# Performance work log

Hardware: AMD Instinct MI355X
Metric: run time of the kernel (lower is better)

## Reference

```python
import jax, jax.numpy as jnp
import numpy as np

N = 50000      # nodes
E = 800000     # edges
G = 64         # graphs in batch
H = 256        # hidden_channels
CE = 128       # coord embed dim = H//2
OTH = 6        # in_channels - 3
ED = 8         # edge_dim
EE = 128       # edge_embedding_dim
GD = 16        # global_dim
L = 3          # num_layers


def setup_inputs() -> dict:
    key = jax.random.key(0)
    ks = jax.random.split(key, 24)
    s = 0.05
    inp = {
        "x": jax.random.normal(ks[0], (N, 9), jnp.float32),
        "edge_index": jax.random.randint(ks[1], (2, E), 0, N),
        "batch": jnp.sort(jax.random.randint(ks[2], (N,), 0, G)),
        "edge_attr": jax.random.normal(ks[3], (E, ED), jnp.float32),
        "global_x": jax.random.normal(ks[4], (G, GD), jnp.float32),
        # coordinate embedder (Linear 3->128 + relu)
        "coord_W": jax.random.normal(ks[5], (3, CE), jnp.float32) * s,
        "coord_b": jnp.zeros((CE,), jnp.float32),
        # node_mlp (Linear 6->128 + relu)
        "node_W": jax.random.normal(ks[6], (OTH, CE), jnp.float32) * s,
        "node_b": jnp.zeros((CE,), jnp.float32),
        # edge processor (Linear 8->128 + relu) and projection 128->256
        "edge_W": jax.random.normal(ks[7], (ED, EE), jnp.float32) * s,
        "edge_b": jnp.zeros((EE,), jnp.float32),
        "proj_W": jax.random.normal(ks[8], (EE, H), jnp.float32) * s,
        "proj_b": jnp.zeros((H,), jnp.float32),
        # stacked GCN layer weights
        "gcn_W": jax.random.normal(ks[9], (L, H, H), jnp.float32) * s,
        "gcn_b": jnp.zeros((L, H), jnp.float32),
        # attention pooling
        "attn_w": jax.random.normal(ks[10], (H,), jnp.float32) * s,
        "attn_b": jnp.zeros((), jnp.float32),
        # global_mlp: Linear 16->256, relu, Linear 256->256
        "gmlp_W1": jax.random.normal(ks[11], (GD, H), jnp.float32) * s,
        "gmlp_b1": jnp.zeros((H,), jnp.float32),
        "gmlp_W2": jax.random.normal(ks[12], (H, H), jnp.float32) * s,
        "gmlp_b2": jnp.zeros((H,), jnp.float32),
        # fc_out: Linear 512->256, relu, Linear 256->1
        "fc_W1": jax.random.normal(ks[13], (2 * H, H), jnp.float32) * s,
        "fc_b1": jnp.zeros((H,), jnp.float32),
        "fc_W2": jax.random.normal(ks[14], (H, 1), jnp.float32) * s,
        "fc_b2": jnp.zeros((1,), jnp.float32),
    }
    return inp


def _segsum(v, idx, num):
    return jax.ops.segment_sum(v, idx, num_segments=num)


def reference(x, edge_index, batch, edge_attr, global_x,
              coord_W, coord_b, node_W, node_b, edge_W, edge_b,
              proj_W, proj_b, gcn_W, gcn_b, attn_w, attn_b,
              gmlp_W1, gmlp_b1, gmlp_W2, gmlp_b2,
              fc_W1, fc_b1, fc_W2, fc_b2):
    relu = jax.nn.relu
    # --- node embedding: coords + other features ---
    coord_emb = relu(x[:, :3] @ coord_W + coord_b)          # [N, 128]
    other_emb = relu(x[:, 3:] @ node_W + node_b)            # [N, 128]
    x_emb = jnp.concatenate([coord_emb, other_emb], axis=1)  # [N, 256]

    # --- edge embedding, aggregated to target nodes (index_add over col) ---
    edge_emb = relu(edge_attr @ edge_W + edge_b) @ proj_W + proj_b  # [E, 256]
    col0 = edge_index[1]
    node_msg = _segsum(edge_emb, col0, N)                    # [N, 256]

    # --- GCN normalization with self-loops ---
    sl = jnp.arange(N)
    row = jnp.concatenate([edge_index[0], sl])
    col = jnp.concatenate([edge_index[1], sl])
    deg = _segsum(jnp.ones_like(col, jnp.float32), col, N)   # >= 1
    dnorm = jax.lax.rsqrt(deg)
    efac = (dnorm[row] * dnorm[col])[:, None]                # [E+N, 1]

    # --- stacked GCN layers (edge messages re-added each layer, per source) ---
    for i in range(L):
        x_in = x_emb + node_msg
        h = x_in @ gcn_W[i]                                  # [N, 256]
        x_emb = _segsum(h[row] * efac, col, N) + gcn_b[i]
        if i < L - 1:
            x_emb = relu(x_emb)

    # --- attention pooling (per-graph softmax over batch index) ---
    scores = x_emb @ attn_w + attn_b                         # [N]
    m = jax.ops.segment_max(scores, batch, num_segments=G)
    e = jnp.exp(scores - m[batch])
    denom = _segsum(e, batch, G)
    attn = e / denom[batch]
    graph_emb = _segsum(x_emb * attn[:, None], batch, G)     # [G, 256]

    # --- global features + head ---
    g = relu(global_x @ gmlp_W1 + gmlp_b1) @ gmlp_W2 + gmlp_b2
    hcat = jnp.concatenate([graph_emb, g], axis=-1)          # [G, 512]
    out = relu(hcat @ fc_W1 + fc_b1) @ fc_W2 + fc_b2         # [G, 1]
    return out
```

## Files before the change

kernel.cpp:

```cpp
#include <hip/hip_runtime.h>


typedef float f32x4 __attribute__((ext_vector_type(4)));
typedef short s16x8 __attribute__((ext_vector_type(8)));

__device__ __forceinline__ unsigned short f2bf(float f) {
  union { float f; unsigned u; } v{f};
  unsigned r = v.u + 0x7fff + ((v.u >> 16) & 1);
  return (unsigned short)(r >> 16);
}
__device__ __forceinline__ float bf2f(unsigned short s) {
  union { unsigned u; float f; } v{(unsigned)s << 16};
  return v.f;
}
__device__ __forceinline__ float blo(unsigned u) {
  union { unsigned x; float f; } v{u << 16};
  return v.f;
}
__device__ __forceinline__ float bhi(unsigned u) {
  union { unsigned x; float f; } v{u & 0xffff0000u};
  return v.f;
}
__device__ __forceinline__ unsigned pk2(float a, float b) {
  return (unsigned)f2bf(a) | ((unsigned)f2bf(b) << 16);
}

__global__ void node_embed_kernel(const float* __restrict__ x,
                                  const float* __restrict__ coord_W, const float* __restrict__ coord_b,
                                  const float* __restrict__ node_W, const float* __restrict__ node_b,
                                  short* __restrict__ x0, int N) {
  int tid = threadIdx.x;
  int node = blockIdx.x * 8 + (tid >> 5);
  if (node >= N) return;
  int ch0 = (tid & 31) * 8;
  const float* xr = x + (size_t)node * 9;
  float a[8];
  if (ch0 < 128) {
    float4 b0 = *(const float4*)&coord_b[ch0];
    float4 b1 = *(const float4*)&coord_b[ch0 + 4];
    a[0]=b0.x; a[1]=b0.y; a[2]=b0.z; a[3]=b0.w; a[4]=b1.x; a[5]=b1.y; a[6]=b1.z; a[7]=b1.w;
#pragma unroll
    for (int k = 0; k < 3; k++) {
      float xv = xr[k];
      float4 w0 = *(const float4*)&coord_W[k * 128 + ch0];
      float4 w1 = *(const float4*)&coord_W[k * 128 + ch0 + 4];
      a[0] = fmaf(xv, w0.x, a[0]); a[1] = fmaf(xv, w0.y, a[1]);
      a[2] = fmaf(xv, w0.z, a[2]); a[3] = fmaf(xv, w0.w, a[3]);
      a[4] = fmaf(xv, w1.x, a[4]); a[5] = fmaf(xv, w1.y, a[5]);
      a[6] = fmaf(xv, w1.z, a[6]); a[7] = fmaf(xv, w1.w, a[7]);
    }
  } else {
    int c0 = ch0 - 128;
    float4 b0 = *(const float4*)&node_b[c0];
    float4 b1 = *(const float4*)&node_b[c0 + 4];
    a[0]=b0.x; a[1]=b0.y; a[2]=b0.z; a[3]=b0.w; a[4]=b1.x; a[5]=b1.y; a[6]=b1.z; a[7]=b1.w;
#pragma unroll
    for (int k = 0; k < 6; k++) {
      float xv = xr[3 + k];
      float4 w0 = *(const float4*)&node_W[k * 128 + c0];
      float4 w1 = *(const float4*)&node_W[k * 128 + c0 + 4];
      a[0] = fmaf(xv, w0.x, a[0]); a[1] = fmaf(xv, w0.y, a[1]);
      a[2] = fmaf(xv, w0.z, a[2]); a[3] = fmaf(xv, w0.w, a[3]);
      a[4] = fmaf(xv, w1.x, a[4]); a[5] = fmaf(xv, w1.y, a[5]);
      a[6] = fmaf(xv, w1.z, a[6]); a[7] = fmaf(xv, w1.w, a[7]);
    }
  }
  uint4 o;
  o.x = pk2(fmaxf(a[0], 0.f), fmaxf(a[1], 0.f));
  o.y = pk2(fmaxf(a[2], 0.f), fmaxf(a[3], 0.f));
  o.z = pk2(fmaxf(a[4], 0.f), fmaxf(a[5], 0.f));
  o.w = pk2(fmaxf(a[6], 0.f), fmaxf(a[7], 0.f));
  *(uint4*)&x0[(size_t)node * 256 + ch0] = o;
}

__global__ void count_kernel(const int* __restrict__ col, int* __restrict__ cnt, int E) {
  int e = blockIdx.x * 256 + threadIdx.x;
  if (e < E) atomicAdd(&cnt[col[e]], 1);
}

__global__ void breduce_kernel(const int* __restrict__ cnt, int* __restrict__ partials, int N) {
  __shared__ int red[256];
  int t = threadIdx.x;
  int i = blockIdx.x * 256 + t;
  int v = (i < N) ? cnt[i] : 0;
  red[t] = v;
  __syncthreads();
  for (int off = 128; off; off >>= 1) {
    if (t < off) red[t] += red[t + off];
    __syncthreads();
  }
  if (t == 0) partials[blockIdx.x] = red[0];
}

__global__ void scan_partials_kernel(int* __restrict__ partials, int nb) {
  __shared__ int s[1024];
  int t = threadIdx.x;
  for (int i = t; i < nb; i += 256) s[i] = partials[i];
  __syncthreads();
  if (t == 0) {
    int run = 0;
    for (int i = 0; i < nb; i++) { int c = s[i]; s[i] = run; run += c; }
  }
  __syncthreads();
  for (int i = t; i < nb; i += 256) partials[i] = s[i];
}

__global__ void scan_apply_kernel(const int* __restrict__ cnt, const int* __restrict__ partials,
                                  int* __restrict__ rowstart, float* __restrict__ dnorm,
                                  int* __restrict__ cursor, int N) {
  __shared__ int red[256];
  int t = threadIdx.x;
  int i = blockIdx.x * 256 + t;
  int v = (i < N) ? cnt[i] : 0;
  red[t] = v;
  __syncthreads();
  for (int off = 1; off < 256; off <<= 1) {
    int x = (t >= off) ? red[t - off] : 0;
    __syncthreads();
    red[t] += x;
    __syncthreads();
  }
  if (i < N) {
    int ex = red[t] - v + partials[blockIdx.x];
    rowstart[i] = ex;
    dnorm[i] = rsqrtf((float)(v + 1));
    cursor[i] = 0;
    if (i == N - 1) rowstart[N] = ex + v;
  }
}

__global__ void scatter_kernel(const int* __restrict__ row, const int* __restrict__ col,
                               const float* __restrict__ edge_attr,
                               const int* __restrict__ rowstart, int* __restrict__ cursor,
                               const float* __restrict__ dnorm,
                               int* __restrict__ csr_row, float* __restrict__ csr_efac,
                               float* __restrict__ ea_sorted, int E) {
  int e = blockIdx.x * 256 + threadIdx.x;
  if (e >= E) return;
  int c = col[e], r = row[e];
  int p = atomicAdd(&cursor[c], 1);
  int slot = rowstart[c] + p;
  csr_row[slot] = r;
  csr_efac[slot] = dnorm[r] * dnorm[c];
  const float4* src = (const float4*)(edge_attr + (size_t)e * 8);
  float4* dst = (float4*)(ea_sorted + (size_t)slot * 8);
  float4 s0 = src[0], s1 = src[1];
  dst[0] = s0;
  dst[1] = s1;
}

__global__ void wt_kernel(const float* __restrict__ gcn_W, const float* __restrict__ proj_W,
                          short* __restrict__ gcnWt, short* __restrict__ projWt) {
  int idx = blockIdx.x * 256 + threadIdx.x;
  if (idx < 3 * 65536) {
    int l = idx >> 16, r = idx & 65535, n = r >> 8, k = r & 255;
    gcnWt[idx] = (short)f2bf(gcn_W[l * 65536 + k * 256 + n]);
  } else {
    int j = idx - 3 * 65536;
    int n = j >> 7, k = j & 127;
    projWt[j] = (short)f2bf(proj_W[k * 256 + n]);
  }
}

__global__ void edge_msg_kernel(const float* __restrict__ ea_sorted,
                                const int* __restrict__ rowstart,
                                const float* __restrict__ edge_W, const float* __restrict__ edge_b,
                                short* __restrict__ msg128, int N) {
  int node = blockIdx.x;
  int ch = threadIdx.x;
  __shared__ float sW[8 * 128];
  __shared__ float sb[128];
  for (int i = ch; i < 8 * 128; i += 128) sW[i] = edge_W[i];
  sb[ch] = edge_b[ch];
  __syncthreads();
  float acc = 0.f;
  int s0 = rowstart[node], s1 = rowstart[node + 1];
  const float4* ea4 = (const float4*)ea_sorted;
  for (int s = s0; s < s1; s++) {
    float4 e0 = ea4[(size_t)s * 2];
    float4 e1 = ea4[(size_t)s * 2 + 1];
    float t = sb[ch];
    t = fmaf(e0.x, sW[0 * 128 + ch], t);
    t = fmaf(e0.y, sW[1 * 128 + ch], t);
    t = fmaf(e0.z, sW[2 * 128 + ch], t);
    t = fmaf(e0.w, sW[3 * 128 + ch], t);
    t = fmaf(e1.x, sW[4 * 128 + ch], t);
    t = fmaf(e1.y, sW[5 * 128 + ch], t);
    t = fmaf(e1.z, sW[6 * 128 + ch], t);
    t = fmaf(e1.w, sW[7 * 128 + ch], t);
    acc += fmaxf(t, 0.f);
  }
  msg128[(size_t)node * 128 + ch] = (short)f2bf(acc);
}

__global__ void __launch_bounds__(256) proj_gemm_mfma(
    const short* __restrict__ msg128, const short* __restrict__ projWt,
    const float* __restrict__ proj_b, const int* __restrict__ cnt,
    const short* __restrict__ x0, float* __restrict__ node_msg,
    short* __restrict__ xin0, int N) {
  __shared__ short As[64][136];
  int tid = threadIdx.x;
  int n0 = blockIdx.x * 64;
  for (int i = tid; i < 64 * 32; i += 256) {
    int r = i >> 5, c4 = (i & 31) << 2;
    int n = n0 + r;
    uint2 v = make_uint2(0, 0);
    if (n < N) v = *(const uint2*)&msg128[(size_t)n * 128 + c4];
    *(uint2*)&As[r][c4] = v;
  }
  __syncthreads();
  int wave = tid >> 6, lane = tid & 63;
  int mrow = wave * 16 + (lane & 15);
  int kgrp = (lane >> 4) * 8;
  f32x4 acc[16];
#pragma unroll
  for (int i = 0; i < 16; i++) acc[i] = (f32x4){0.f, 0.f, 0.f, 0.f};
  const short* wbase = projWt + (size_t)(lane & 15) * 128 + kgrp;
#pragma unroll
  for (int kk = 0; kk < 4; kk++) {
    s16x8 a = *(const s16x8*)&As[mrow][kk * 32 + kgrp];
#pragma unroll
    for (int nf = 0; nf < 16; nf++) {
      s16x8 b = *(const s16x8*)&wbase[(size_t)nf * 16 * 128 + kk * 32];
      acc[nf] = __builtin_amdgcn_mfma_f32_16x16x32_bf16(a, b, acc[nf], 0, 0, 0);
    }
  }
  int orow0 = wave * 16 + (lane >> 4) * 4;
  int ocol = lane & 15;
#pragma unroll
  for (int nf = 0; nf < 16; nf++) {
    int c = nf * 16 + ocol;
    float pb = proj_b[c];
#pragma unroll
    for (int r = 0; r < 4; r++) {
      int n = n0 + orow0 + r;
      if (n < N) {
        float v = acc[nf][r] + (float)cnt[n] * pb;
        node_msg[(size_t)n * 256 + c] = v;
        xin0[(size_t)n * 256 + c] =
            (short)f2bf(v + bf2f((unsigned short)x0[(size_t)n * 256 + c]));
      }
    }
  }
}

__global__ void __launch_bounds__(256) gcn_gemm_mfma(
    const short* __restrict__ Xin, const short* __restrict__ Wt,
    short* __restrict__ Hout, int N) {
  __shared__ short As[64][264];
  int tid = threadIdx.x;
  int n0 = blockIdx.x * 64;
  for (int i = tid; i < 64 * 64; i += 256) {
    int r = i >> 6, c4 = (i & 63) << 2;
    int n = n0 + r;
    uint2 v = make_uint2(0, 0);
    if (n < N) v = *(const uint2*)&Xin[(size_t)n * 256 + c4];
    *(uint2*)&As[r][c4] = v;
  }
  __syncthreads();
  int wave = tid >> 6, lane = tid & 63;
  int mrow = wave * 16 + (lane & 15);
  int kgrp = (lane >> 4) * 8;
  f32x4 acc[16];
#pragma unroll
  for (int i = 0; i < 16; i++) acc[i] = (f32x4){0.f, 0.f, 0.f, 0.f};
  const short* wbase = Wt + (size_t)(lane & 15) * 256 + kgrp;
#pragma unroll
  for (int kk = 0; kk < 8; kk++) {
    s16x8 a = *(const s16x8*)&As[mrow][kk * 32 + kgrp];
#pragma unroll
    for (int nf = 0; nf < 16; nf++) {
      s16x8 b = *(const s16x8*)&wbase[(size_t)nf * 16 * 256 + kk * 32];
      acc[nf] = __builtin_amdgcn_mfma_f32_16x16x32_bf16(a, b, acc[nf], 0, 0, 0);
    }
  }
  int orow0 = wave * 16 + (lane >> 4) * 4;
  int ocol = lane & 15;
#pragma unroll
  for (int nf = 0; nf < 16; nf++) {
#pragma unroll
    for (int r = 0; r < 4; r++) {
      int n = n0 + orow0 + r;
      if (n < N) Hout[(size_t)n * 256 + nf * 16 + ocol] = (short)f2bf(acc[nf][r]);
    }
  }
}

__global__ void __launch_bounds__(256) gcn_agg_kernel(
    const short* __restrict__ h, const int* __restrict__ csr_row,
    const float* __restrict__ csr_efac, const int* __restrict__ rowstart,
    const float* __restrict__ dnorm, const float* __restrict__ b,
    const float* __restrict__ node_msg, short* __restrict__ xin,
    float* __restrict__ x_emb, const float* __restrict__ attn_w,
    const float* __restrict__ attn_b, float* __restrict__ scores,
    int last, int N) {
  int lane = threadIdx.x & 63;
  int node = blockIdx.x * 4 + (threadIdx.x >> 6);
  if (node >= N) return;
  int ch0 = lane << 2;
  size_t rowb = (size_t)node * 256 + ch0;
  float dn = dnorm[node];
  float w = dn * dn;
  uint2 hv = *(const uint2*)&h[rowb];
  float a0 = blo(hv.x) * w, a1 = bhi(hv.x) * w;
  float a2 = blo(hv.y) * w, a3 = bhi(hv.y) * w;
  int s = rowstart[node], s1 = rowstart[node + 1];
  for (; s + 4 <= s1; s += 4) {
    int r0 = csr_row[s], r1 = csr_row[s + 1], r2 = csr_row[s + 2], r3 = csr_row[s + 3];
    float f0 = csr_efac[s], f1 = csr_efac[s + 1], f2 = csr_efac[s + 2], f3 = csr_efac[s + 3];
    uint2 v0 = *(const uint2*)&h[(size_t)r0 * 256 + ch0];
    uint2 v1 = *(const uint2*)&h[(size_t)r1 * 256 + ch0];
    uint2 v2 = *(const uint2*)&h[(size_t)r2 * 256 + ch0];
    uint2 v3 = *(const uint2*)&h[(size_t)r3 * 256 + ch0];
    a0 = fmaf(blo(v0.x), f0, a0); a1 = fmaf(bhi(v0.x), f0, a1);
    a2 = fmaf(blo(v0.y), f0, a2); a3 = fmaf(bhi(v0.y), f0, a3);
    a0 = fmaf(blo(v1.x), f1, a0); a1 = fmaf(bhi(v1.x), f1, a1);
    a2 = fmaf(blo(v1.y), f1, a2); a3 = fmaf(bhi(v1.y), f1, a3);
    a0 = fmaf(blo(v2.x), f2, a0); a1 = fmaf(bhi(v2.x), f2, a1);
    a2 = fmaf(blo(v2.y), f2, a2); a3 = fmaf(bhi(v2.y), f2, a3);
    a0 = fmaf(blo(v3.x), f3, a0); a1 = fmaf(bhi(v3.x), f3, a1);
    a2 = fmaf(blo(v3.y), f3, a2); a3 = fmaf(bhi(v3.y), f3, a3);
  }
  for (; s < s1; s++) {
    int r = csr_row[s];
    float f = csr_efac[s];
    uint2 v = *(const uint2*)&h[(size_t)r * 256 + ch0];
    a0 = fmaf(blo(v.x), f, a0); a1 = fmaf(bhi(v.x), f, a1);
    a2 = fmaf(blo(v.y), f, a2); a3 = fmaf(bhi(v.y), f, a3);
  }
  float4 bv = *(const float4*)&b[ch0];
  a0 += bv.x; a1 += bv.y; a2 += bv.z; a3 += bv.w;
  if (!last) {
    float4 mv = *(const float4*)&node_msg[rowb];
    float y0 = fmaxf(a0, 0.f) + mv.x;
    float y1 = fmaxf(a1, 0.f) + mv.y;
    float y2 = fmaxf(a2, 0.f) + mv.z;
    float y3 = fmaxf(a3, 0.f) + mv.w;
    uint2 o;
    o.x = pk2(y0, y1);
    o.y = pk2(y2, y3);
    *(uint2*)&xin[rowb] = o;
  } else {
    *(float4*)&x_emb[rowb] = make_float4(a0, a1, a2, a3);
    float4 aw = *(const float4*)&attn_w[ch0];
    float p = a0 * aw.x + a1 * aw.y + a2 * aw.z + a3 * aw.w;
#pragma unroll
    for (int off = 32; off; off >>= 1) p += __shfl_down(p, off);
    if (lane == 0) scores[node] = p + attn_b[0];
  }
}

__global__ void gse_kernel(const int* __restrict__ batch, int* __restrict__ gs,
                           int* __restrict__ ge, int N) {
  int i = blockIdx.x * 256 + threadIdx.x;
  if (i >= N) return;
  int g = batch[i];
  if (i == 0) gs[g] = 0;
  else {
    int gp = batch[i - 1];
    if (gp != g) { gs[g] = i; ge[gp] = i - 1; }
  }
  if (i == N - 1) ge[g] = N - 1;
}

__global__ void softmax_kernel(const float* __restrict__ scores, const int* __restrict__ gs,
                               const int* __restrict__ ge, float* __restrict__ wnode) {
  int g = blockIdx.x;
  int tid = threadIdx.x;
  __shared__ float red[256];
  int s0 = gs[g], e1 = ge[g];
  if (s0 > e1) return;
  int s1 = e1 + 1;
  float m = -1e30f;
  for (int i = s0 + tid; i < s1; i += 256) m = fmaxf(m, scores[i]);
  red[tid] = m;
  __syncthreads();
  for (int off = 128; off; off >>= 1) {
    if (tid < off) red[tid] = fmaxf(red[tid], red[tid + off]);
    __syncthreads();
  }
  m = red[0];
  __syncthreads();
  float d = 0.f;
  for (int i = s0 + tid; i < s1; i += 256) d += expf(scores[i] - m);
  red[tid] = d;
  __syncthreads();
  for (int off = 128; off; off >>= 1) {
    if (tid < off) red[tid] += red[tid + off];
    __syncthreads();
  }
  float rd = 1.f / red[0];
  for (int i = s0 + tid; i < s1; i += 256) wnode[i] = expf(scores[i] - m) * rd;
}

__global__ void __launch_bounds__(256) pool_sum_kernel(
    const float* __restrict__ x_emb, const float* __restrict__ wnode,
    const int* __restrict__ batch, float* __restrict__ graph_emb, int N) {
  __shared__ int sb[256];
  __shared__ float sw[256];
  int ch = threadIdx.x;
  int i0 = blockIdx.x * 256;
  int lim = min(256, N - i0);
  if (ch < lim) { sb[ch] = batch[i0 + ch]; sw[ch] = wnode[i0 + ch]; }
  __syncthreads();
  int curg = sb[0];
  float acc = 0.f;
  for (int j = 0; j < lim; j++) {
    int g = sb[j];
    if (g != curg) {
      atomicAdd(&graph_emb[(size_t)curg * 256 + ch], acc);
      acc = 0.f;
      curg = g;
    }
    acc = fmaf(x_emb[(size_t)(i0 + j) * 256 + ch], sw[j], acc);
  }
  atomicAdd(&graph_emb[(size_t)curg * 256 + ch], acc);
}

__global__ void head_kernel(const float* __restrict__ global_x, const float* __restrict__ graph_emb,
                            const float* __restrict__ W1, const float* __restrict__ b1,
                            const float* __restrict__ W2, const float* __restrict__ b2,
                            const float* __restrict__ fW1, const float* __restrict__ fb1,
                            const float* __restrict__ fW2, const float* __restrict__ fb2,
                            float* __restrict__ out) {
  int g = blockIdx.x;
  int ch = threadIdx.x;
  __shared__ float t1[256], g2s[256], t3s[256];
  float a = b1[ch];
  const float* gx = global_x + g * 16;
#pragma unroll
  for (int k = 0; k < 16; k++) a = fmaf(gx[k], W1[k * 256 + ch], a);
  t1[ch] = fmaxf(a, 0.f);
  __syncthreads();
  float bb = b2[ch];
  for (int k = 0; k < 256; k++) bb = fmaf(t1[k], W2[k * 256 + ch], bb);
  g2s[ch] = bb;
  __syncthreads();
  float c = fb1[ch];
  const float* ger = graph_emb + (size_t)g * 256;
  for (int k = 0; k < 256; k++) c = fmaf(ger[k], fW1[k * 256 + ch], c);
  for (int k = 0; k < 256; k++) c = fmaf(g2s[k], fW1[(256 + k) * 256 + ch], c);
  t3s[ch] = fmaxf(c, 0.f);
  __syncthreads();
  t1[ch] = t3s[ch] * fW2[ch];
  __syncthreads();
  for (int off = 128; off; off >>= 1) {
    if (ch < off) t1[ch] += t1[ch + off];
    __syncthreads();
  }
  if (ch == 0) out[g] = t1[0] + fb2[0];
}

extern "C" void kernel_launch(void* const* d_in, const int* in_sizes, int n_in,
                              void* d_out, int out_size, void* d_ws, size_t ws_size,
                              hipStream_t stream) {
  const float* x        = (const float*)d_in[0];
  const int*   ei       = (const int*)d_in[1];
  const int*   batch    = (const int*)d_in[2];
  const float* edge_attr= (const float*)d_in[3];
  const float* global_x = (const float*)d_in[4];
  const float* coord_W  = (const float*)d_in[5];
  const float* coord_b  = (const float*)d_in[6];
  const float* node_W   = (const float*)d_in[7];
  const float* node_b   = (const float*)d_in[8];
  const float* edge_W   = (const float*)d_in[9];
  const float* edge_b   = (const float*)d_in[10];
  const float* proj_W   = (const float*)d_in[11];
  const float* proj_b   = (const float*)d_in[12];
  const float* gcn_W    = (const float*)d_in[13];
  const float* gcn_b    = (const float*)d_in[14];
  const float* attn_w   = (const float*)d_in[15];
  const float* attn_b   = (const float*)d_in[16];
  const float* gmlp_W1  = (const float*)d_in[17];
  const float* gmlp_b1  = (const float*)d_in[18];
  const float* gmlp_W2  = (const float*)d_in[19];
  const float* gmlp_b2  = (const float*)d_in[20];
  const float* fc_W1    = (const float*)d_in[21];
  const float* fc_b1    = (const float*)d_in[22];
  const float* fc_W2    = (const float*)d_in[23];
  const float* fc_b2    = (const float*)d_in[24];

  const int N = in_sizes[0] / 9;
  const int E = in_sizes[3] / 8;
  const int G = in_sizes[4] / 16;
  const int NB = (N + 255) / 256;

  char* w = (char*)d_ws;
  auto alloc = [&](size_t bytes) -> char* {
    char* p = w;
    w += (bytes + 255) & ~(size_t)255;
    return p;
  };
  float* node_msg = (float*)alloc((size_t)N * 256 * 4);
  short* xin      = (short*)alloc((size_t)N * 256 * 2);
  short* h        = (short*)alloc((size_t)N * 256 * 2);
  short* x0       = (short*)alloc((size_t)N * 256 * 2);
  float* big      = (float*)alloc((size_t)N * 256 * 4);
  short* msg128   = h;
  float* ea_sorted= big;
  float* x_emb    = big;
  short* gcnWt    = (short*)alloc((size_t)3 * 65536 * 2);
  short* projWt   = (short*)alloc((size_t)256 * 128 * 2);
  int*   cnt      = (int*)alloc((size_t)N * 4);
  int*   rowstart = (int*)alloc((size_t)(N + 1) * 4);
  int*   cursor   = (int*)alloc((size_t)N * 4);
  float* dnorm    = (float*)alloc((size_t)N * 4);
  int*   csr_row  = (int*)alloc((size_t)E * 4);
  float* csr_efac = (float*)alloc((size_t)E * 4);
  float* scores   = (float*)alloc((size_t)N * 4);
  float* wnode    = (float*)alloc((size_t)N * 4);
  int*   partials = (int*)alloc((size_t)NB * 4);
  int*   gs       = (int*)alloc((size_t)G * 4);
  int*   ge       = (int*)alloc((size_t)G * 4);
  float* graph_emb= (float*)alloc((size_t)G * 256 * 4);

  hipMemsetAsync(cnt, 0, (size_t)N * 4, stream);
  hipMemsetAsync(gs, 0x7f, (size_t)G * 4, stream);
  hipMemsetAsync(ge, 0xff, (size_t)G * 4, stream);
  hipMemsetAsync(graph_emb, 0, (size_t)G * 256 * 4, stream);

  wt_kernel<<<(3 * 65536 + 256 * 128 + 255) / 256, 256, 0, stream>>>(gcn_W, proj_W, gcnWt, projWt);
  node_embed_kernel<<<(N + 7) / 8, 256, 0, stream>>>(
      x, coord_W, coord_b, node_W, node_b, x0, N);
  count_kernel<<<(E + 255) / 256, 256, 0, stream>>>(ei + E, cnt, E);
  breduce_kernel<<<NB, 256, 0, stream>>>(cnt, partials, N);
  scan_partials_kernel<<<1, 256, 0, stream>>>(partials, NB);
  scan_apply_kernel<<<NB, 256, 0, stream>>>(cnt, partials, rowstart, dnorm, cursor, N);
  scatter_kernel<<<(E + 255) / 256, 256, 0, stream>>>(
      ei, ei + E, edge_attr, rowstart, cursor, dnorm, csr_row, csr_efac, ea_sorted, E);
  edge_msg_kernel<<<N, 128, 0, stream>>>(ea_sorted, rowstart, edge_W, edge_b, msg128, N);
  proj_gemm_mfma<<<(N + 63) / 64, 256, 0, stream>>>(
      msg128, projWt, proj_b, cnt, x0, node_msg, xin, N);
  for (int l = 0; l < 3; l++) {
    gcn_gemm_mfma<<<(N + 63) / 64, 256, 0, stream>>>(
        xin, gcnWt + (size_t)l * 65536, h, N);
    gcn_agg_kernel<<<(N + 3) / 4, 256, 0, stream>>>(
        h, csr_row, csr_efac, rowstart, dnorm, gcn_b + (size_t)l * 256,
        node_msg, xin, x_emb, attn_w, attn_b, scores, (l == 2) ? 1 : 0, N);
  }
  gse_kernel<<<(N + 255) / 256, 256, 0, stream>>>(batch, gs, ge, N);
  softmax_kernel<<<G, 256, 0, stream>>>(scores, gs, ge, wnode);
  pool_sum_kernel<<<NB, 256, 0, stream>>>(x_emb, wnode, batch, graph_emb, N);
  head_kernel<<<G, 256, 0, stream>>>(global_x, graph_emb, gmlp_W1, gmlp_b1, gmlp_W2, gmlp_b2,
                                     fc_W1, fc_b1, fc_W2, fc_b2, (float*)d_out);
}
```

Baseline: 957.5 us.

## Fuse GCN aggregation into next layer's GEMM and pack CSR edge records

Each GCN layer's neighbor aggregation, bias, relu and node-message add now fills the shared-memory A tile that feeds the next layer's MFMA GEMM. The first GCN GEMM is folded into the projection kernel, which removes the round trip of the xin activation through global memory and cuts launches. CSR edge data is packed into one int4 record (edge id, source, norm factor), and edge_msg now gathers edge_attr by id instead of reading a presorted copy. node_msg and x_emb are stored as bf16, lowering bandwidth at some precision cost. The fused layer kernel runs the aggregation with 64-node blocks where each wave walks 16 nodes serially, so parallelism and latency hiding during the gather may drop.

```diff
diff --git a/kernel.cpp b/kernel.cpp
--- a/kernel.cpp
+++ b/kernel.cpp
@@ -130,23 +130,15 @@
 }
 
 __global__ void scatter_kernel(const int* __restrict__ row, const int* __restrict__ col,
-                               const float* __restrict__ edge_attr,
                                const int* __restrict__ rowstart, int* __restrict__ cursor,
                                const float* __restrict__ dnorm,
-                               int* __restrict__ csr_row, float* __restrict__ csr_efac,
-                               float* __restrict__ ea_sorted, int E) {
+                               int4* __restrict__ pk, int E) {
   int e = blockIdx.x * 256 + threadIdx.x;
   if (e >= E) return;
   int c = col[e], r = row[e];
   int p = atomicAdd(&cursor[c], 1);
   int slot = rowstart[c] + p;
-  csr_row[slot] = r;
-  csr_efac[slot] = dnorm[r] * dnorm[c];
-  const float4* src = (const float4*)(edge_attr + (size_t)e * 8);
-  float4* dst = (float4*)(ea_sorted + (size_t)slot * 8);
-  float4 s0 = src[0], s1 = src[1];
-  dst[0] = s0;
-  dst[1] = s1;
+  pk[slot] = make_int4(e, r, __float_as_int(dnorm[r] * dnorm[c]), 0);
 }
 
 __global__ void wt_kernel(const float* __restrict__ gcn_W, const float* __restrict__ proj_W,
@@ -162,7 +154,8 @@
   }
 }
 
-__global__ void edge_msg_kernel(const float* __restrict__ ea_sorted,
+__global__ void edge_msg_kernel(const float* __restrict__ edge_attr,
+                                const int4* __restrict__ pk,
                                 const int* __restrict__ rowstart,
                                 const float* __restrict__ edge_W, const float* __restrict__ edge_b,
                                 short* __restrict__ msg128, int N) {
@@ -175,10 +168,10 @@
   __syncthreads();
   float acc = 0.f;
   int s0 = rowstart[node], s1 = rowstart[node + 1];
-  const float4* ea4 = (const float4*)ea_sorted;
   for (int s = s0; s < s1; s++) {
-    float4 e0 = ea4[(size_t)s * 2];
-    float4 e1 = ea4[(size_t)s * 2 + 1];
+    int eid = pk[s].x;
+    const float4* ea = (const float4*)(edge_attr + (size_t)eid * 8);
+    float4 e0 = ea[0], e1 = ea[1];
     float t = sb[ch];
     t = fmaf(e0.x, sW[0 * 128 + ch], t);
     t = fmaf(e0.y, sW[1 * 128 + ch], t);
@@ -193,12 +186,13 @@
   msg128[(size_t)node * 128 + ch] = (short)f2bf(acc);
 }
 
-__global__ void __launch_bounds__(256) proj_gemm_mfma(
+__global__ void __launch_bounds__(256) fused_proj_gemm(
     const short* __restrict__ msg128, const short* __restrict__ projWt,
     const float* __restrict__ proj_b, const int* __restrict__ cnt,
-    const short* __restrict__ x0, float* __restrict__ node_msg,
-    short* __restrict__ xin0, int N) {
+    const short* __restrict__ x0, const short* __restrict__ W0t,
+    short* __restrict__ node_msg, short* __restrict__ hout, int N) {
   __shared__ short As[64][136];
+  __shared__ short Xs[64][264];
   int tid = threadIdx.x;
   int n0 = blockIdx.x * 64;
   for (int i = tid; i < 64 * 32; i += 256) {
@@ -215,50 +209,123 @@
   f32x4 acc[16];
 #pragma unroll
   for (int i = 0; i < 16; i++) acc[i] = (f32x4){0.f, 0.f, 0.f, 0.f};
-  const short* wbase = projWt + (size_t)(lane & 15) * 128 + kgrp;
-#pragma unroll
-  for (int kk = 0; kk < 4; kk++) {
-    s16x8 a = *(const s16x8*)&As[mrow][kk * 32 + kgrp];
-#pragma unroll
-    for (int nf = 0; nf < 16; nf++) {
-      s16x8 b = *(const s16x8*)&wbase[(size_t)nf * 16 * 128 + kk * 32];
-      acc[nf] = __builtin_amdgcn_mfma_f32_16x16x32_bf16(a, b, acc[nf], 0, 0, 0);
+  {
+    const short* wbase = projWt + (size_t)(lane & 15) * 128 + kgrp;
+#pragma unroll
+    for (int kk = 0; kk < 4; kk++) {
+      s16x8 a = *(const s16x8*)&As[mrow][kk * 32 + kgrp];
+#pragma unroll
+      for (int nf = 0; nf < 16; nf++) {
+        s16x8 b = *(const s16x8*)&wbase[(size_t)nf * 16 * 128 + kk * 32];
+        acc[nf] = __builtin_amdgcn_mfma_f32_16x16x32_bf16(a, b, acc[nf], 0, 0, 0);
+      }
     }
   }
   int orow0 = wave * 16 + (lane >> 4) * 4;
   int ocol = lane & 15;
 #pragma unroll
+  for (int r = 0; r < 4; r++) {
+    int i = orow0 + r;
+    int n = n0 + i;
+    if (n < N) {
+      float cn = (float)cnt[n];
+#pragma unroll
+      for (int nf = 0; nf < 16; nf++) {
+        int c = nf * 16 + ocol;
+        float v = acc[nf][r] + cn * proj_b[c];
+        unsigned short nm = f2bf(v);
+        node_msg[(size_t)n * 256 + c] = (short)nm;
+        Xs[i][c] = (short)f2bf(bf2f(nm) + bf2f((unsigned short)x0[(size_t)n * 256 + c]));
+      }
+    } else {
+#pragma unroll
+      for (int nf = 0; nf < 16; nf++) Xs[i][nf * 16 + ocol] = 0;
+    }
+  }
+  __syncthreads();
+#pragma unroll
+  for (int i = 0; i < 16; i++) acc[i] = (f32x4){0.f, 0.f, 0.f, 0.f};
+  {
+    const short* wbase = W0t + (size_t)(lane & 15) * 256 + kgrp;
+#pragma unroll
+    for (int kk = 0; kk < 8; kk++) {
+      s16x8 a = *(const s16x8*)&Xs[mrow][kk * 32 + kgrp];
+#pragma unroll
+      for (int nf = 0; nf < 16; nf++) {
+        s16x8 b = *(const s16x8*)&wbase[(size_t)nf * 16 * 256 + kk * 32];
+        acc[nf] = __builtin_amdgcn_mfma_f32_16x16x32_bf16(a, b, acc[nf], 0, 0, 0);
+      }
+    }
+  }
+#pragma unroll
   for (int nf = 0; nf < 16; nf++) {
-    int c = nf * 16 + ocol;
-    float pb = proj_b[c];
 #pragma unroll
     for (int r = 0; r < 4; r++) {
       int n = n0 + orow0 + r;
-      if (n < N) {
-        float v = acc[nf][r] + (float)cnt[n] * pb;
-        node_msg[(size_t)n * 256 + c] = v;
-        xin0[(size_t)n * 256 + c] =
-            (short)f2bf(v + bf2f((unsigned short)x0[(size_t)n * 256 + c]));
-      }
-    }
-  }
-}
-
-__global__ void __launch_bounds__(256) gcn_gemm_mfma(
-    const short* __restrict__ Xin, const short* __restrict__ Wt,
-    short* __restrict__ Hout, int N) {
-  __shared__ short As[64][264];
+      if (n < N) hout[(size_t)n * 256 + nf * 16 + ocol] = (short)f2bf(acc[nf][r]);
+    }
+  }
+}
+
+__global__ void __launch_bounds__(256) fused_layer(
+    const short* __restrict__ hprev, const int4* __restrict__ pk,
+    const int* __restrict__ rowstart, const float* __restrict__ dnorm,
+    const float* __restrict__ bprev, const short* __restrict__ node_msg,
+    const short* __restrict__ Wt, short* __restrict__ hnext, int N) {
+  __shared__ short Xs[64][264];
   int tid = threadIdx.x;
   int n0 = blockIdx.x * 64;
-  for (int i = tid; i < 64 * 64; i += 256) {
-    int r = i >> 6, c4 = (i & 63) << 2;
-    int n = n0 + r;
-    uint2 v = make_uint2(0, 0);
-    if (n < N) v = *(const uint2*)&Xin[(size_t)n * 256 + c4];
-    *(uint2*)&As[r][c4] = v;
-  }
-  __syncthreads();
   int wave = tid >> 6, lane = tid & 63;
+  int ch0 = lane << 2;
+  float4 bv = *(const float4*)&bprev[ch0];
+  for (int i = wave * 16; i < wave * 16 + 16; i++) {
+    int n = n0 + i;
+    if (n >= N) {
+      *(uint2*)&Xs[i][ch0] = make_uint2(0, 0);
+      continue;
+    }
+    size_t rowb = (size_t)n * 256 + ch0;
+    float dn = dnorm[n];
+    float wgt = dn * dn;
+    uint2 hv = *(const uint2*)&hprev[rowb];
+    float a0 = blo(hv.x) * wgt, a1 = bhi(hv.x) * wgt;
+    float a2 = blo(hv.y) * wgt, a3 = bhi(hv.y) * wgt;
+    int s = rowstart[n], s1 = rowstart[n + 1];
+    for (; s + 4 <= s1; s += 4) {
+      int4 p0 = pk[s], p1 = pk[s + 1], p2 = pk[s + 2], p3 = pk[s + 3];
+      float f0 = __int_as_float(p0.z), f1 = __int_as_float(p1.z);
+      float f2 = __int_as_float(p2.z), f3 = __int_as_float(p3.z);
+      uint2 v0 = *(const uint2*)&hprev[(size_t)p0.y * 256 + ch0];
+      uint2 v1 = *(const uint2*)&hprev[(size_t)p1.y * 256 + ch0];
+      uint2 v2 = *(const uint2*)&hprev[(size_t)p2.y * 256 + ch0];
+      uint2 v3 = *(const uint2*)&hprev[(size_t)p3.y * 256 + ch0];
+      a0 = fmaf(blo(v0.x), f0, a0); a1 = fmaf(bhi(v0.x), f0, a1);
+      a2 = fmaf(blo(v0.y), f0, a2); a3 = fmaf(bhi(v0.y), f0, a3);
+      a0 = fmaf(blo(v1.x), f1, a0); a1 = fmaf(bhi(v1.x), f1, a1);
+      a2 = fmaf(blo(v1.y), f1, a2); a3 = fmaf(bhi(v1.y), f1, a3);
+      a0 = fmaf(blo(v2.x), f2, a0); a1 = fmaf(bhi(v2.x), f2, a1);
+      a2 = fmaf(blo(v2.y), f2, a2); a3 = fmaf(bhi(v2.y), f2, a3);
+      a0 = fmaf(blo(v3.x), f3, a0); a1 = fmaf(bhi(v3.x), f3, a1);
+      a2 = fmaf(blo(v3.y), f3, a2); a3 = fmaf(bhi(v3.y), f3, a3);
+    }
+    for (; s < s1; s++) {
+      int4 p = pk[s];
+      float f = __int_as_float(p.z);
+      uint2 v = *(const uint2*)&hprev[(size_t)p.y * 256 + ch0];
+      a0 = fmaf(blo(v.x), f, a0); a1 = fmaf(bhi(v.x), f, a1);
+      a2 = fmaf(blo(v.y), f, a2); a3 = fmaf(bhi(v.y), f, a3);
+    }
+    uint2 mv = *(const uint2*)&node_msg[rowb];
+    float y0 = fmaxf(a0 + bv.x, 0.f) + blo(mv.x);
+    float y1 = fmaxf(a1 + bv.y, 0.f) + bhi(mv.x);
+    float y2 = fmaxf(a2 + bv.z, 0.f) + blo(mv.y);
+    float y3 = fmaxf(a3 + bv.w, 0.f) + bhi(mv.y);
+    uint2 o;
+    o.x = pk2(y0, y1);
+    o.y = pk2(y2, y3);
+    *(uint2*)&Xs[i][ch0] = o;
+  }
+  __syncthreads();
   int mrow = wave * 16 + (lane & 15);
   int kgrp = (lane >> 4) * 8;
   f32x4 acc[16];
@@ -267,7 +334,7 @@
   const short* wbase = Wt + (size_t)(lane & 15) * 256 + kgrp;
 #pragma unroll
   for (int kk = 0; kk < 8; kk++) {
-    s16x8 a = *(const s16x8*)&As[mrow][kk * 32 + kgrp];
+    s16x8 a = *(const s16x8*)&Xs[mrow][kk * 32 + kgrp];
 #pragma unroll
     for (int nf = 0; nf < 16; nf++) {
       s16x8 b = *(const s16x8*)&wbase[(size_t)nf * 16 * 256 + kk * 32];
@@ -281,37 +348,36 @@
 #pragma unroll
     for (int r = 0; r < 4; r++) {
       int n = n0 + orow0 + r;
-      if (n < N) Hout[(size_t)n * 256 + nf * 16 + ocol] = (short)f2bf(acc[nf][r]);
-    }
-  }
-}
-
-__global__ void __launch_bounds__(256) gcn_agg_kernel(
-    const short* __restrict__ h, const int* __restrict__ csr_row,
-    const float* __restrict__ csr_efac, const int* __restrict__ rowstart,
-    const float* __restrict__ dnorm, const float* __restrict__ b,
-    const float* __restrict__ node_msg, short* __restrict__ xin,
-    float* __restrict__ x_emb, const float* __restrict__ attn_w,
-    const float* __restrict__ attn_b, float* __restrict__ scores,
-    int last, int N) {
+      if (n < N) hnext[(size_t)n * 256 + nf * 16 + ocol] = (short)f2bf(acc[nf][r]);
+    }
+  }
+}
+
+__global__ void __launch_bounds__(256) final_agg_kernel(
+    const short* __restrict__ h, const int4* __restrict__ pk,
+    const int* __restrict__ rowstart, const float* __restrict__ dnorm,
+    const float* __restrict__ b, short* __restrict__ x_emb,
+    const float* __restrict__ attn_w, const float* __restrict__ attn_b,
+    float* __restrict__ scores, int N) {
   int lane = threadIdx.x & 63;
   int node = blockIdx.x * 4 + (threadIdx.x >> 6);
   if (node >= N) return;
   int ch0 = lane << 2;
   size_t rowb = (size_t)node * 256 + ch0;
   float dn = dnorm[node];
-  float w = dn * dn;
+  float wgt = dn * dn;
   uint2 hv = *(const uint2*)&h[rowb];
-  float a0 = blo(hv.x) * w, a1 = bhi(hv.x) * w;
-  float a2 = blo(hv.y) * w, a3 = bhi(hv.y) * w;
+  float a0 = blo(hv.x) * wgt, a1 = bhi(hv.x) * wgt;
+  float a2 = blo(hv.y) * wgt, a3 = bhi(hv.y) * wgt;
   int s = rowstart[node], s1 = rowstart[node + 1];
   for (; s + 4 <= s1; s += 4) {
-    int r0 = csr_row[s], r1 = csr_row[s + 1], r2 = csr_row[s + 2], r3 = csr_row[s + 3];
-    float f0 = csr_efac[s], f1 = csr_efac[s + 1], f2 = csr_efac[s + 2], f3 = csr_efac[s + 3];
-    uint2 v0 = *(const uint2*)&h[(size_t)r0 * 256 + ch0];
-    uint2 v1 = *(const uint2*)&h[(size_t)r1 * 256 + ch0];
-    uint2 v2 = *(const uint2*)&h[(size_t)r2 * 256 + ch0];
-    uint2 v3 = *(const uint2*)&h[(size_t)r3 * 256 + ch0];
+    int4 p0 = pk[s], p1 = pk[s + 1], p2 = pk[s + 2], p3 = pk[s + 3];
+    float f0 = __int_as_float(p0.z), f1 = __int_as_float(p1.z);
+    float f2 = __int_as_float(p2.z), f3 = __int_as_float(p3.z);
+    uint2 v0 = *(const uint2*)&h[(size_t)p0.y * 256 + ch0];
+    uint2 v1 = *(const uint2*)&h[(size_t)p1.y * 256 + ch0];
+    uint2 v2 = *(const uint2*)&h[(size_t)p2.y * 256 + ch0];
+    uint2 v3 = *(const uint2*)&h[(size_t)p3.y * 256 + ch0];
     a0 = fmaf(blo(v0.x), f0, a0); a1 = fmaf(bhi(v0.x), f0, a1);
     a2 = fmaf(blo(v0.y), f0, a2); a3 = fmaf(bhi(v0.y), f0, a3);
     a0 = fmaf(blo(v1.x), f1, a0); a1 = fmaf(bhi(v1.x), f1, a1);
@@ -322,32 +388,23 @@
     a2 = fmaf(blo(v3.y), f3, a2); a3 = fmaf(bhi(v3.y), f3, a3);
   }
   for (; s < s1; s++) {
-    int r = csr_row[s];
-    float f = csr_efac[s];
-    uint2 v = *(const uint2*)&h[(size_t)r * 256 + ch0];
+    int4 p = pk[s];
+    float f = __int_as_float(p.z);
+    uint2 v = *(const uint2*)&h[(size_t)p.y * 256 + ch0];
     a0 = fmaf(blo(v.x), f, a0); a1 = fmaf(bhi(v.x), f, a1);
     a2 = fmaf(blo(v.y), f, a2); a3 = fmaf(bhi(v.y), f, a3);
   }
   float4 bv = *(const float4*)&b[ch0];
   a0 += bv.x; a1 += bv.y; a2 += bv.z; a3 += bv.w;
-  if (!last) {
-    float4 mv = *(const float4*)&node_msg[rowb];
-    float y0 = fmaxf(a0, 0.f) + mv.x;
-    float y1 = fmaxf(a1, 0.f) + mv.y;
-    float y2 = fmaxf(a2, 0.f) + mv.z;
-    float y3 = fmaxf(a3, 0.f) + mv.w;
-    uint2 o;
-    o.x = pk2(y0, y1);
-    o.y = pk2(y2, y3);
-    *(uint2*)&xin[rowb] = o;
-  } else {
-    *(float4*)&x_emb[rowb] = make_float4(a0, a1, a2, a3);
-    float4 aw = *(const float4*)&attn_w[ch0];
-    float p = a0 * aw.x + a1 * aw.y + a2 * aw.z + a3 * aw.w;
-#pragma unroll
-    for (int off = 32; off; off >>= 1) p += __shfl_down(p, off);
-    if (lane == 0) scores[node] = p + attn_b[0];
-  }
+  uint2 o;
+  o.x = pk2(a0, a1);
+  o.y = pk2(a2, a3);
+  *(uint2*)&x_emb[rowb] = o;
+  float4 aw = *(const float4*)&attn_w[ch0];
+  float p = a0 * aw.x + a1 * aw.y + a2 * aw.z + a3 * aw.w;
+#pragma unroll
+  for (int off = 32; off; off >>= 1) p += __shfl_down(p, off);
+  if (lane == 0) scores[node] = p + attn_b[0];
 }
 
 __global__ void gse_kernel(const int* __restrict__ batch, int* __restrict__ gs,
@@ -394,7 +451,7 @@
 }
 
 __global__ void __launch_bounds__(256) pool_sum_kernel(
-    const float* __restrict__ x_emb, const float* __restrict__ wnode,
+    const short* __restrict__ x_emb, const float* __restrict__ wnode,
     const int* __restrict__ batch, float* __restrict__ graph_emb, int N) {
   __shared__ int sb[256];
   __shared__ float sw[256];
@@ -412,7 +469,7 @@
       acc = 0.f;
       curg = g;
     }
-    acc = fmaf(x_emb[(size_t)(i0 + j) * 256 + ch], sw[j], acc);
+    acc = fmaf(bf2f((unsigned short)x_emb[(size_t)(i0 + j) * 256 + ch]), sw[j], acc);
   }
   atomicAdd(&graph_emb[(size_t)curg * 256 + ch], acc);
 }
@@ -491,22 +548,19 @@
     w += (bytes + 255) & ~(size_t)255;
     return p;
   };
-  float* node_msg = (float*)alloc((size_t)N * 256 * 4);
-  short* xin      = (short*)alloc((size_t)N * 256 * 2);
-  short* h        = (short*)alloc((size_t)N * 256 * 2);
   short* x0       = (short*)alloc((size_t)N * 256 * 2);
-  float* big      = (float*)alloc((size_t)N * 256 * 4);
-  short* msg128   = h;
-  float* ea_sorted= big;
-  float* x_emb    = big;
+  short* node_msg = (short*)alloc((size_t)N * 256 * 2);
+  short* hA       = (short*)alloc((size_t)N * 256 * 2);
+  short* hB       = (short*)alloc((size_t)N * 256 * 2);
+  short* x_emb    = (short*)alloc((size_t)N * 256 * 2);
+  short* msg128   = x_emb;
+  int4*  pk       = (int4*)alloc((size_t)E * 16);
   short* gcnWt    = (short*)alloc((size_t)3 * 65536 * 2);
   short* projWt   = (short*)alloc((size_t)256 * 128 * 2);
   int*   cnt      = (int*)alloc((size_t)N * 4);
   int*   rowstart = (int*)alloc((size_t)(N + 1) * 4);
   int*   cursor   = (int*)alloc((size_t)N * 4);
   float* dnorm    = (float*)alloc((size_t)N * 4);
-  int*   csr_row  = (int*)alloc((size_t)E * 4);
-  float* csr_efac = (float*)alloc((size_t)E * 4);
   float* scores   = (float*)alloc((size_t)N * 4);
   float* wnode    = (float*)alloc((size_t)N * 4);
   int*   partials = (int*)alloc((size_t)NB * 4);
@@ -527,17 +581,16 @@
   scan_partials_kernel<<<1, 256, 0, stream>>>(partials, NB);
   scan_apply_kernel<<<NB, 256, 0, stream>>>(cnt, partials, rowstart, dnorm, cursor, N);
   scatter_kernel<<<(E + 255) / 256, 256, 0, stream>>>(
-      ei, ei + E, edge_attr, rowstart, cursor, dnorm, csr_row, csr_efac, ea_sorted, E);
-  edge_msg_kernel<<<N, 128, 0, stream>>>(ea_sorted, rowstart, edge_W, edge_b, msg128, N);
-  proj_gemm_mfma<<<(N + 63) / 64, 256, 0, stream>>>(
-      msg128, projWt, proj_b, cnt, x0, node_msg, xin, N);
-  for (int l = 0; l < 3; l++) {
-    gcn_gemm_mfma<<<(N + 63) / 64, 256, 0, stream>>>(
-        xin, gcnWt + (size_t)l * 65536, h, N);
-    gcn_agg_kernel<<<(N + 3) / 4, 256, 0, stream>>>(
-        h, csr_row, csr_efac, rowstart, dnorm, gcn_b + (size_t)l * 256,
-        node_msg, xin, x_emb, attn_w, attn_b, scores, (l == 2) ? 1 : 0, N);
-  }
+      ei, ei + E, rowstart, cursor, dnorm, pk, E);
+  edge_msg_kernel<<<N, 128, 0, stream>>>(edge_attr, pk, rowstart, edge_W, edge_b, msg128, N);
+  fused_proj_gemm<<<(N + 63) / 64, 256, 0, stream>>>(
+      msg128, projWt, proj_b, cnt, x0, gcnWt, node_msg, hA, N);
+  fused_layer<<<(N + 63) / 64, 256, 0, stream>>>(
+      hA, pk, rowstart, dnorm, gcn_b, node_msg, gcnWt + 65536, hB, N);
+  fused_layer<<<(N + 63) / 64, 256, 0, stream>>>(
+      hB, pk, rowstart, dnorm, gcn_b + 256, node_msg, gcnWt + 2 * 65536, hA, N);
+  final_agg_kernel<<<(N + 3) / 4, 256, 0, stream>>>(
+      hA, pk, rowstart, dnorm, gcn_b + 512, x_emb, attn_w, attn_b, scores, N);
   gse_kernel<<<(N + 255) / 256, 256, 0, stream>>>(batch, gs, ge, N);
   softmax_kernel<<<G, 256, 0, stream>>>(scores, gs, ge, wnode);
   pool_sum_kernel<<<NB, 256, 0, stream>>>(x_emb, wnode, batch, graph_emb, N);
```

Result: slower. 1.055 ms (+10.2%).
